# Optimization experiments

Measured on AMD Instinct MI355X. Metric: run time of the kernel, lower is better.

The kernel has to match this reference:

```python
import jax, jax.numpy as jnp
import numpy as np

EPS = 1e-5

def setup_inputs() -> dict:
    key = jax.random.key(0)
    k1, k2, k3 = jax.random.split(key, 3)
    B, T, F = 64, 512, 1024
    x = jax.random.normal(k1, (B, T, F), dtype=jnp.float32)
    # Linear(width_time, width_time): torch stores weight as (out, in)
    W = jax.random.normal(k2, (T, T), dtype=jnp.float32) * (1.0 / np.sqrt(T))
    b = jax.random.normal(k3, (T,), dtype=jnp.float32) * 0.01
    gamma = jnp.ones((1,), dtype=jnp.float32)
    beta = jnp.zeros((1,), dtype=jnp.float32)
    return {"x": x, "W": W, "b": b, "gamma": gamma, "beta": beta}


def reference(x, W, b, gamma, beta):
    # TSBatchNorm2d: BatchNorm2d(num_features=1) over x.unsqueeze(1)
    # -> stats over all (B, T, F) elements, scalar affine (training-mode batch stats).
    mean = jnp.mean(x)
    var = jnp.var(x)
    y = (x - mean) * jax.lax.rsqrt(var + EPS) * gamma[0] + beta[0]
    # transpose (B,T,F) -> (B,F,T), Linear over time dim, ReLU
    # (dropout is identity in eval mode), transpose back, residual add.
    yt = jnp.swapaxes(y, 1, 2)                      # (B, F, T)
    h = jnp.einsum('bft,ut->bfu', yt, W) + b        # Linear: y @ W.T + b
    h = jax.nn.relu(h)
    return x + jnp.swapaxes(h, 1, 2)                # (B, T, F)
```

## Files before the change

kernel.cpp:

```cpp
#include <hip/hip_runtime.h>
#include <stdint.h>

#define TDIM 512
#define FDIM 1024
#define NTOT 33554432.0f
#define EPS  1e-5f

typedef unsigned short ushort_t;
typedef unsigned short ushort4_t __attribute__((ext_vector_type(4)));
typedef short short8 __attribute__((ext_vector_type(8)));
typedef float floatx4 __attribute__((ext_vector_type(4)));

__device__ __forceinline__ ushort_t f2bf(float f) {
    union { float f; uint32_t u; } v; v.f = f;
    uint32_t r = (v.u + 0x7fffu + ((v.u >> 16) & 1u)) >> 16;
    return (ushort_t)r;
}

__device__ __forceinline__ void async16(const ushort_t* g, ushort_t* l) {
    __builtin_amdgcn_global_load_lds(
        (const __attribute__((address_space(1))) void*)g,
        (__attribute__((address_space(3))) void*)l, 16, 0, 0);
}


__global__ __launch_bounds__(256) void k_stats_transpose(
    const float* __restrict__ x, ushort_t* __restrict__ xTC,
    float2* __restrict__ partials)
{
    __shared__ ushort_t tile[64 * 128];
    __shared__ float red[8];

    int tid = threadIdx.x, bid = blockIdx.x;
    int b  = bid >> 6;
    int t0 = ((bid >> 3) & 7) << 6;
    int ft = bid & 7;
    int f0 = ft << 7;

    int r8 = tid >> 5, c8 = tid & 31;
    const float* xb = x + ((size_t)(b * TDIM + t0) * FDIM) + f0;

    float4 v[8];
#pragma unroll
    for (int p = 0; p < 8; ++p)
        v[p] = *(const float4*)(xb + (size_t)(p * 8 + r8) * FDIM + c8 * 4);

    float s = 0.f, q = 0.f;
#pragma unroll
    for (int p = 0; p < 8; ++p) {
        float4 t = v[p];
        s += t.x + t.y + t.z + t.w;
        q += t.x * t.x + t.y * t.y + t.z * t.z + t.w * t.w;
        ushort4_t pk;
        pk[0] = f2bf(t.x); pk[1] = f2bf(t.y); pk[2] = f2bf(t.z); pk[3] = f2bf(t.w);
        *(ushort4_t*)&tile[(p * 8 + r8) * 128 + c8 * 4] = pk;
    }

#pragma unroll
    for (int off = 32; off > 0; off >>= 1) {
        s += __shfl_down(s, off, 64);
        q += __shfl_down(q, off, 64);
    }
    int lane = tid & 63, w = tid >> 6;
    if (lane == 0) { red[w] = s; red[4 + w] = q; }
    __syncthreads();
    if (tid == 0) {
        partials[bid] = make_float2(red[0] + red[1] + red[2] + red[3],
                                    red[4] + red[5] + red[6] + red[7]);
    }

    int fl = tid & 127, hf = tid >> 7;
    size_t base = ((size_t)((b * 8 + ft) * 16) + (t0 >> 5) + hf) * 4096;
#pragma unroll
    for (int qq = 0; qq < 4; ++qq) {
        int tr = hf * 32 + qq * 8;
        uint32_t w0 = (uint32_t)tile[(tr + 0) * 128 + fl] | ((uint32_t)tile[(tr + 1) * 128 + fl] << 16);
        uint32_t w1 = (uint32_t)tile[(tr + 2) * 128 + fl] | ((uint32_t)tile[(tr + 3) * 128 + fl] << 16);
        uint32_t w2 = (uint32_t)tile[(tr + 4) * 128 + fl] | ((uint32_t)tile[(tr + 5) * 128 + fl] << 16);
        uint32_t w3 = (uint32_t)tile[(tr + 6) * 128 + fl] | ((uint32_t)tile[(tr + 7) * 128 + fl] << 16);
        uint4 o = make_uint4(w0, w1, w2, w3);
        *(uint4*)&xTC[base + (size_t)(qq * 128 + fl) * 8] = o;
    }
}

__global__ __launch_bounds__(256) void k_wcast(
    const float* __restrict__ W, ushort_t* __restrict__ WbC,
    float* __restrict__ rowsumW)
{
    __shared__ float red[4];
    int u = blockIdx.x, tid = threadIdx.x;
    float2 lv = *(const float2*)(W + (size_t)u * 512 + 2 * tid);

    int mt = u >> 7, m = u & 127;
    int kt = tid >> 4;
    int qq = (tid & 15) >> 2;
    int e  = 2 * (tid & 3);
    size_t off = ((size_t)(mt * 16 + kt)) * 4096 + (size_t)(qq * 128 + m) * 8 + e;
    uint32_t pk = (uint32_t)f2bf(lv.x) | ((uint32_t)f2bf(lv.y) << 16);
    *(uint32_t*)&WbC[off] = pk;

    float s = lv.x + lv.y;
#pragma unroll
    for (int off2 = 32; off2 > 0; off2 >>= 1) s += __shfl_down(s, off2, 64);
    int lane = tid & 63, w = tid >> 6;
    if (lane == 0) red[w] = s;
    __syncthreads();
    if (tid == 0) rowsumW[u] = red[0] + red[1] + red[2] + red[3];
}

__global__ __launch_bounds__(256) void k_reduce(
    const float2* __restrict__ partials, const float* __restrict__ rowsumW,
    const float* __restrict__ bias, const float* __restrict__ gamma,
    const float* __restrict__ beta, float* __restrict__ stats,
    float* __restrict__ d)
{
    __shared__ float red[8];
    __shared__ float sac[2];
    int tid = threadIdx.x;
    float s = 0.f, q = 0.f;
#pragma unroll
    for (int i = 0; i < 16; ++i) {
        float2 p = partials[i * 256 + tid];
        s += p.x; q += p.y;
    }
#pragma unroll
    for (int off = 32; off > 0; off >>= 1) {
        s += __shfl_down(s, off, 64);
        q += __shfl_down(q, off, 64);
    }
    int lane = tid & 63, w = tid >> 6;
    if (lane == 0) { red[w] = s; red[4 + w] = q; }
    __syncthreads();
    if (tid == 0) {
        float S = red[0] + red[1] + red[2] + red[3];
        float Q = red[4] + red[5] + red[6] + red[7];
        float mean = S * (1.f / NTOT);
        float var  = Q * (1.f / NTOT) - mean * mean;
        float a    = gamma[0] * rsqrtf(var + EPS);
        float c    = beta[0] - mean * a;
        stats[0] = a;
        sac[0] = a; sac[1] = c;
    }
    __syncthreads();
    float c = sac[1];
    d[tid]       = c * rowsumW[tid]       + bias[tid];
    d[tid + 256] = c * rowsumW[tid + 256] + bias[tid + 256];
}

__global__ __launch_bounds__(256) void k_gemm(
    const ushort_t* __restrict__ WbC, const ushort_t* __restrict__ xTC,
    const float* __restrict__ x, const float* __restrict__ d,
    const float* __restrict__ stats, float* __restrict__ out)
{
    __shared__ ulong smem_raw[6144];
    ushort_t* lds  = (ushort_t*)smem_raw;
    float*    ldsC = (float*)smem_raw;

    int tid = threadIdx.x;
    int w = tid >> 6, lane = tid & 63;

    int hb   = blockIdx.x;
    int xcd  = hb & 7;
    int rr   = hb >> 3;
    int mt   = rr & 3;
    int nt   = ((rr >> 2) << 3) + xcd;
    int b = nt >> 3, ft = nt & 7;

    int wr = w >> 1, wc = w & 1;
    int l15 = lane & 15, q = lane >> 4;

    const ushort_t* Ab = WbC + (size_t)mt * 16 * 4096 + tid * 8;
    const ushort_t* Bb = xTC + (size_t)(b * 8 + ft) * 16 * 4096 + tid * 8;

    floatx4 acc[4][4] = {};

    auto stage = [&](int kt, int s) {
        const ushort_t* Ag = Ab + kt * 4096;
        const ushort_t* Bg = Bb + kt * 4096;
        ushort_t* ls = lds + s * 8192;
        async16(Ag,        &ls[tid * 8]);
        async16(Ag + 2048, &ls[2048 + tid * 8]);
        async16(Bg,        &ls[4096 + tid * 8]);
        async16(Bg + 2048, &ls[4096 + 2048 + tid * 8]);
    };

    stage(0, 0);
    stage(1, 1);

#pragma unroll
    for (int kt = 0; kt < 16; ++kt) {
        if (kt < 14) {
            stage(kt + 2, (kt + 2) % 3);
            asm volatile("s_waitcnt vmcnt(8)" ::: "memory");
        } else if (kt == 14) {
            asm volatile("s_waitcnt vmcnt(4)" ::: "memory");
        } else {
            asm volatile("s_waitcnt vmcnt(0)" ::: "memory");
        }
        __builtin_amdgcn_s_barrier();

        const ushort_t* cA = lds + (kt % 3) * 8192;
        const ushort_t* cB = cA + 4096;
        short8 af[4], bfr[4];
#pragma unroll
        for (int i = 0; i < 4; ++i) {
            int m = wr * 64 + i * 16 + l15;
            af[i] = *(const short8*)&cA[(q * 128 + m) * 8];
        }
#pragma unroll
        for (int j = 0; j < 4; ++j) {
            int n = wc * 64 + j * 16 + l15;
            bfr[j] = *(const short8*)&cB[(q * 128 + n) * 8];
        }
        asm volatile("s_waitcnt lgkmcnt(0)" ::: "memory");
        __builtin_amdgcn_s_barrier();

#pragma unroll
        for (int i = 0; i < 4; ++i)
#pragma unroll
            for (int j = 0; j < 4; ++j)
                acc[i][j] = __builtin_amdgcn_mfma_f32_16x16x32_bf16(
                    af[i], bfr[j], acc[i][j], 0, 0, 0);
    }

    __syncthreads();

    float a = stats[0];
    int row = tid >> 3, cs = (tid & 7) * 16;
#pragma unroll
    for (int p = 0; p < 4; ++p) {
        if (wr == (p >> 1)) {
#pragma unroll
            for (int ii = 0; ii < 2; ++ii) {
                int i = (p & 1) * 2 + ii;
                int rl0 = i * 16 + q * 4 - (p & 1) * 32;
#pragma unroll
                for (int j = 0; j < 4; ++j) {
                    int col = wc * 64 + j * 16 + l15;
#pragma unroll
                    for (int r = 0; r < 4; ++r)
                        ldsC[(rl0 + r) * 132 + col] = acc[i][j][r];
                }
            }
        }
        __syncthreads();
        int tg = mt * 128 + p * 32 + row;
        float dt = d[tg];
        size_t gbase = ((size_t)b * TDIM + tg) * FDIM + ft * 128 + cs;
        const float* xr = x + gbase;
        float* orow = out + gbase;
#pragma unroll
        for (int k4 = 0; k4 < 4; ++k4) {
            float4 xv = *(const float4*)(xr + k4 * 4);
            float4 cv = *(const float4*)&ldsC[row * 132 + cs + k4 * 4];
            float4 o;
            o.x = xv.x + fmaxf(a * cv.x + dt, 0.f);
            o.y = xv.y + fmaxf(a * cv.y + dt, 0.f);
            o.z = xv.z + fmaxf(a * cv.z + dt, 0.f);
            o.w = xv.w + fmaxf(a * cv.w + dt, 0.f);
            *(float4*)(orow + k4 * 4) = o;
        }
        __syncthreads();
    }
}

extern "C" void kernel_launch(void* const* d_in, const int* in_sizes, int n_in,
                              void* d_out, int out_size, void* d_ws, size_t ws_size,
                              hipStream_t stream) {
    const float* x     = (const float*)d_in[0];
    const float* W     = (const float*)d_in[1];
    const float* bias  = (const float*)d_in[2];
    const float* gamma = (const float*)d_in[3];
    const float* beta  = (const float*)d_in[4];
    float* out = (float*)d_out;

    char* ws = (char*)d_ws;
    float*    stats    = (float*)ws;
    float*    dvec     = (float*)(ws + 1024);
    float*    rowsumW  = (float*)(ws + 4096);
    float2*   partials = (float2*)(ws + 8192);
    ushort_t* WbC      = (ushort_t*)(ws + (64 << 10));
    ushort_t* xTC      = (ushort_t*)(ws + (1 << 20));

    k_stats_transpose<<<4096, 256, 0, stream>>>(x, xTC, partials);
    k_wcast<<<512, 256, 0, stream>>>(W, WbC, rowsumW);
    k_reduce<<<1, 256, 0, stream>>>(partials, rowsumW, bias, gamma, beta, stats, dvec);
    k_gemm<<<2048, 256, 0, stream>>>(WbC, xTC, x, dvec, stats, out);
}
```

Measured before the change: 315.5 us.

## Drop bf16 transposed x copy; GEMM loads fp32 x directly with swizzled LDS

Removes the transpose-and-cast pass that wrote a bf16 transposed copy of x, so the stats kernel only reduces sums, and merges the W cast into the same launch. The GEMM now streams fp32 x tiles straight into LDS with an XOR swizzle and converts to bf16 while building MFMA fragments, switching from a 3-stage to a 2-stage pipeline because the tiles grew. This saves a full write plus re-read of the intermediate, but doubles B-tile bytes per GEMM load, adds per-element conversion and scalar LDS reads in the inner loop, and shortens the prefetch depth.

```diff
diff --git a/kernel.cpp b/kernel.cpp
--- a/kernel.cpp
+++ b/kernel.cpp
@@ -17,95 +17,60 @@
     return (ushort_t)r;
 }
 
-__device__ __forceinline__ void async16(const ushort_t* g, ushort_t* l) {
+__device__ __forceinline__ void async16(const void* g, void* l) {
     __builtin_amdgcn_global_load_lds(
         (const __attribute__((address_space(1))) void*)g,
         (__attribute__((address_space(3))) void*)l, 16, 0, 0);
 }
 
-
-__global__ __launch_bounds__(256) void k_stats_transpose(
-    const float* __restrict__ x, ushort_t* __restrict__ xTC,
+__global__ __launch_bounds__(256) void k_statsW(
+    const float* __restrict__ x, const float* __restrict__ W,
+    ushort_t* __restrict__ WbC, float* __restrict__ rowsumW,
     float2* __restrict__ partials)
 {
-    __shared__ ushort_t tile[64 * 128];
     __shared__ float red[8];
-
     int tid = threadIdx.x, bid = blockIdx.x;
-    int b  = bid >> 6;
-    int t0 = ((bid >> 3) & 7) << 6;
-    int ft = bid & 7;
-    int f0 = ft << 7;
-
-    int r8 = tid >> 5, c8 = tid & 31;
-    const float* xb = x + ((size_t)(b * TDIM + t0) * FDIM) + f0;
-
-    float4 v[8];
-#pragma unroll
-    for (int p = 0; p < 8; ++p)
-        v[p] = *(const float4*)(xb + (size_t)(p * 8 + r8) * FDIM + c8 * 4);
-
-    float s = 0.f, q = 0.f;
-#pragma unroll
-    for (int p = 0; p < 8; ++p) {
-        float4 t = v[p];
-        s += t.x + t.y + t.z + t.w;
-        q += t.x * t.x + t.y * t.y + t.z * t.z + t.w * t.w;
-        ushort4_t pk;
-        pk[0] = f2bf(t.x); pk[1] = f2bf(t.y); pk[2] = f2bf(t.z); pk[3] = f2bf(t.w);
-        *(ushort4_t*)&tile[(p * 8 + r8) * 128 + c8 * 4] = pk;
-    }
-
-#pragma unroll
-    for (int off = 32; off > 0; off >>= 1) {
-        s += __shfl_down(s, off, 64);
-        q += __shfl_down(q, off, 64);
-    }
     int lane = tid & 63, w = tid >> 6;
-    if (lane == 0) { red[w] = s; red[4 + w] = q; }
-    __syncthreads();
-    if (tid == 0) {
-        partials[bid] = make_float2(red[0] + red[1] + red[2] + red[3],
-                                    red[4] + red[5] + red[6] + red[7]);
-    }
-
-    int fl = tid & 127, hf = tid >> 7;
-    size_t base = ((size_t)((b * 8 + ft) * 16) + (t0 >> 5) + hf) * 4096;
-#pragma unroll
-    for (int qq = 0; qq < 4; ++qq) {
-        int tr = hf * 32 + qq * 8;
-        uint32_t w0 = (uint32_t)tile[(tr + 0) * 128 + fl] | ((uint32_t)tile[(tr + 1) * 128 + fl] << 16);
-        uint32_t w1 = (uint32_t)tile[(tr + 2) * 128 + fl] | ((uint32_t)tile[(tr + 3) * 128 + fl] << 16);
-        uint32_t w2 = (uint32_t)tile[(tr + 4) * 128 + fl] | ((uint32_t)tile[(tr + 5) * 128 + fl] << 16);
-        uint32_t w3 = (uint32_t)tile[(tr + 6) * 128 + fl] | ((uint32_t)tile[(tr + 7) * 128 + fl] << 16);
-        uint4 o = make_uint4(w0, w1, w2, w3);
-        *(uint4*)&xTC[base + (size_t)(qq * 128 + fl) * 8] = o;
-    }
-}
-
-__global__ __launch_bounds__(256) void k_wcast(
-    const float* __restrict__ W, ushort_t* __restrict__ WbC,
-    float* __restrict__ rowsumW)
-{
-    __shared__ float red[4];
-    int u = blockIdx.x, tid = threadIdx.x;
-    float2 lv = *(const float2*)(W + (size_t)u * 512 + 2 * tid);
-
-    int mt = u >> 7, m = u & 127;
-    int kt = tid >> 4;
-    int qq = (tid & 15) >> 2;
-    int e  = 2 * (tid & 3);
-    size_t off = ((size_t)(mt * 16 + kt)) * 4096 + (size_t)(qq * 128 + m) * 8 + e;
-    uint32_t pk = (uint32_t)f2bf(lv.x) | ((uint32_t)f2bf(lv.y) << 16);
-    *(uint32_t*)&WbC[off] = pk;
-
-    float s = lv.x + lv.y;
-#pragma unroll
-    for (int off2 = 32; off2 > 0; off2 >>= 1) s += __shfl_down(s, off2, 64);
-    int lane = tid & 63, w = tid >> 6;
-    if (lane == 0) red[w] = s;
-    __syncthreads();
-    if (tid == 0) rowsumW[u] = red[0] + red[1] + red[2] + red[3];
+
+    if (bid < 4096) {
+        const float* xb = x + (size_t)bid * 8192;
+        float s = 0.f, q = 0.f;
+#pragma unroll
+        for (int p = 0; p < 8; ++p) {
+            float4 t = *(const float4*)(xb + p * 1024 + tid * 4);
+            s += t.x + t.y + t.z + t.w;
+            q += t.x * t.x + t.y * t.y + t.z * t.z + t.w * t.w;
+        }
+#pragma unroll
+        for (int off = 32; off > 0; off >>= 1) {
+            s += __shfl_down(s, off, 64);
+            q += __shfl_down(q, off, 64);
+        }
+        if (lane == 0) { red[w] = s; red[4 + w] = q; }
+        __syncthreads();
+        if (tid == 0) {
+            partials[bid] = make_float2(red[0] + red[1] + red[2] + red[3],
+                                        red[4] + red[5] + red[6] + red[7]);
+        }
+    } else {
+        int u = bid - 4096;
+        float2 lv = *(const float2*)(W + (size_t)u * 512 + 2 * tid);
+
+        int mt = u >> 7, m = u & 127;
+        int kt = tid >> 4;
+        int qq = (tid & 15) >> 2;
+        int e  = 2 * (tid & 3);
+        size_t off = ((size_t)(mt * 16 + kt)) * 4096 + (size_t)(qq * 128 + m) * 8 + e;
+        uint32_t pk = (uint32_t)f2bf(lv.x) | ((uint32_t)f2bf(lv.y) << 16);
+        *(uint32_t*)&WbC[off] = pk;
+
+        float s = lv.x + lv.y;
+#pragma unroll
+        for (int off2 = 32; off2 > 0; off2 >>= 1) s += __shfl_down(s, off2, 64);
+        if (lane == 0) red[w] = s;
+        __syncthreads();
+        if (tid == 0) rowsumW[u] = red[0] + red[1] + red[2] + red[3];
+    }
 }
 
 __global__ __launch_bounds__(256) void k_reduce(
@@ -148,13 +113,13 @@
 }
 
 __global__ __launch_bounds__(256) void k_gemm(
-    const ushort_t* __restrict__ WbC, const ushort_t* __restrict__ xTC,
-    const float* __restrict__ x, const float* __restrict__ d,
-    const float* __restrict__ stats, float* __restrict__ out)
+    const ushort_t* __restrict__ WbC, const float* __restrict__ x,
+    const float* __restrict__ d, const float* __restrict__ stats,
+    float* __restrict__ out)
 {
     __shared__ ulong smem_raw[6144];
-    ushort_t* lds  = (ushort_t*)smem_raw;
-    float*    ldsC = (float*)smem_raw;
+    char*  lds  = (char*)smem_raw;
+    float* ldsC = (float*)smem_raw;
 
     int tid = threadIdx.x;
     int w = tid >> 6, lane = tid & 63;
@@ -170,37 +135,48 @@
     int l15 = lane & 15, q = lane >> 4;
 
     const ushort_t* Ab = WbC + (size_t)mt * 16 * 4096 + tid * 8;
-    const ushort_t* Bb = xTC + (size_t)(b * 8 + ft) * 16 * 4096 + tid * 8;
+
+    const float* Bs[4];
+    {
+        int tl0 = tid >> 5, fx = (tid & 31) * 4;
+#pragma unroll
+        for (int c = 0; c < 4; ++c) {
+            int tl = tl0 + c * 8;
+            int f  = fx ^ (((tl >> 3) & 3) << 3);
+            Bs[c] = x + ((size_t)b * TDIM + tl) * FDIM + ft * 128 + f;
+        }
+    }
 
     floatx4 acc[4][4] = {};
 
     auto stage = [&](int kt, int s) {
+        char* ls = lds + s * 24576;
         const ushort_t* Ag = Ab + kt * 4096;
-        const ushort_t* Bg = Bb + kt * 4096;
-        ushort_t* ls = lds + s * 8192;
-        async16(Ag,        &ls[tid * 8]);
-        async16(Ag + 2048, &ls[2048 + tid * 8]);
-        async16(Bg,        &ls[4096 + tid * 8]);
-        async16(Bg + 2048, &ls[4096 + 2048 + tid * 8]);
+        async16(Ag,        ls + tid * 16);
+        async16(Ag + 2048, ls + 4096 + tid * 16);
+        char* lb = ls + 8192;
+        size_t koff = (size_t)kt * 32 * FDIM;
+#pragma unroll
+        for (int c = 0; c < 4; ++c)
+            async16(Bs[c] + koff, lb + c * 4096 + tid * 16);
     };
 
     stage(0, 0);
-    stage(1, 1);
 
 #pragma unroll
     for (int kt = 0; kt < 16; ++kt) {
-        if (kt < 14) {
-            stage(kt + 2, (kt + 2) % 3);
-            asm volatile("s_waitcnt vmcnt(8)" ::: "memory");
-        } else if (kt == 14) {
-            asm volatile("s_waitcnt vmcnt(4)" ::: "memory");
+        if (kt < 15) {
+            stage(kt + 1, (kt + 1) & 1);
+            asm volatile("s_waitcnt vmcnt(6)" ::: "memory");
         } else {
             asm volatile("s_waitcnt vmcnt(0)" ::: "memory");
         }
         __builtin_amdgcn_s_barrier();
 
-        const ushort_t* cA = lds + (kt % 3) * 8192;
-        const ushort_t* cB = cA + 4096;
+        char* ls = lds + (kt & 1) * 24576;
+        const ushort_t* cA = (const ushort_t*)ls;
+        const float*    cB = (const float*)(ls + 8192);
+
         short8 af[4], bfr[4];
 #pragma unroll
         for (int i = 0; i < 4; ++i) {
@@ -209,8 +185,15 @@
         }
 #pragma unroll
         for (int j = 0; j < 4; ++j) {
-            int n = wc * 64 + j * 16 + l15;
-            bfr[j] = *(const short8*)&cB[(q * 128 + n) * 8];
+            int fxr = (wc * 64 + j * 16 + l15) ^ (q << 3);
+            float xv[8];
+#pragma unroll
+            for (int e = 0; e < 8; ++e)
+                xv[e] = cB[(q * 8 + e) * 128 + fxr];
+            short8 bv;
+#pragma unroll
+            for (int e = 0; e < 8; ++e) bv[e] = (short)f2bf(xv[e]);
+            bfr[j] = bv;
         }
         asm volatile("s_waitcnt lgkmcnt(0)" ::: "memory");
         __builtin_amdgcn_s_barrier();
@@ -280,10 +263,8 @@
     float*    rowsumW  = (float*)(ws + 4096);
     float2*   partials = (float2*)(ws + 8192);
     ushort_t* WbC      = (ushort_t*)(ws + (64 << 10));
-    ushort_t* xTC      = (ushort_t*)(ws + (1 << 20));
-
-    k_stats_transpose<<<4096, 256, 0, stream>>>(x, xTC, partials);
-    k_wcast<<<512, 256, 0, stream>>>(W, WbC, rowsumW);
+
+    k_statsW<<<4608, 256, 0, stream>>>(x, W, WbC, rowsumW, partials);
     k_reduce<<<1, 256, 0, stream>>>(partials, rowsumW, bias, gamma, beta, stats, dvec);
-    k_gemm<<<2048, 256, 0, stream>>>(WbC, xTC, x, dvec, stats, out);
-}
+    k_gemm<<<2048, 256, 0, stream>>>(WbC, x, dvec, stats, out);
+}
```

Measured after the change: 326.1 us. 3.4% more time.
